# Optimization experiments

Measured on AMD Instinct MI355X. Metric: run time of the kernel, lower is better.

The kernel has to match this reference:

```python
import jax, jax.numpy as jnp
import numpy as np

D_MODEL = 256
N_HEAD = 8
D_FF = 1024
B = 8
N_PER = 4096
NQ = B * N_PER
L = 16
NEG_INF = -1e9
EPS = 1e-5


def layer_norm(x, g, b):
    mu = jnp.mean(x, axis=-1, keepdims=True)
    var = jnp.mean(jnp.square(x - mu), axis=-1, keepdims=True)
    return (x - mu) * jax.lax.rsqrt(var + EPS) * g + b


def setup_inputs() -> dict:
    key = jax.random.key(0)
    ks = jax.random.split(key, 20)
    s = 1.0 / np.sqrt(D_MODEL)
    sf = 1.0 / np.sqrt(D_FF)
    inp = {
        "src": jax.random.normal(ks[0], (NQ, D_MODEL), jnp.float32),
        "pos": jax.random.normal(ks[1], (NQ, D_MODEL), jnp.float32),
        # per-batch-relative neighbor indices in [-1, N_PER); -1 == invalid/padded
        "index_pair": jax.random.randint(ks[2], (NQ, L), 0, N_PER + 1, jnp.int32) - 1,
        "query_batch_cnt": jnp.full((B,), N_PER, jnp.int32),
        "key_batch_cnt": jnp.full((B,), N_PER, jnp.int32),
        "index_pair_batch": (jnp.arange(NQ, dtype=jnp.int32) // N_PER).astype(jnp.int32),
        "Wq": jax.random.normal(ks[3], (D_MODEL, D_MODEL), jnp.float32) * s,
        "bq": jnp.zeros((D_MODEL,), jnp.float32),
        "Wk": jax.random.normal(ks[4], (D_MODEL, D_MODEL), jnp.float32) * s,
        "bk": jnp.zeros((D_MODEL,), jnp.float32),
        "Wv": jax.random.normal(ks[5], (D_MODEL, D_MODEL), jnp.float32) * s,
        "bv": jnp.zeros((D_MODEL,), jnp.float32),
        "Wo": jax.random.normal(ks[6], (D_MODEL, D_MODEL), jnp.float32) * s,
        "bo": jnp.zeros((D_MODEL,), jnp.float32),
        "W1": jax.random.normal(ks[7], (D_MODEL, D_FF), jnp.float32) * s,
        "b1": jnp.zeros((D_FF,), jnp.float32),
        "W2": jax.random.normal(ks[8], (D_FF, D_MODEL), jnp.float32) * sf,
        "b2": jnp.zeros((D_MODEL,), jnp.float32),
        "g1": jnp.ones((D_MODEL,), jnp.float32),
        "be1": jnp.zeros((D_MODEL,), jnp.float32),
        "g2": jnp.ones((D_MODEL,), jnp.float32),
        "be2": jnp.zeros((D_MODEL,), jnp.float32),
    }
    return inp


def local_attn(q, k, v, index_pair, key_batch_cnt, index_pair_batch,
               Wq, bq, Wk, bk, Wv, bv, Wo, bo):
    H, hd = N_HEAD, D_MODEL // N_HEAD
    scale = 1.0 / np.sqrt(hd)
    qh = (q @ Wq + bq).reshape(NQ, H, hd) * scale        # [Nq,H,hd]
    kh = (k @ Wk + bk).reshape(NQ, H, hd)                # [Nk,H,hd] (Nk==Nq)
    vh = (v @ Wv + bv).reshape(NQ, H, hd)
    # start offset of each batch's keys in the stacked key tensor
    offs = jnp.cumsum(key_batch_cnt) - key_batch_cnt      # [B]
    valid = index_pair >= 0                               # [Nq,L]
    gidx = jnp.where(valid, index_pair + offs[index_pair_batch][:, None], 0)
    k_g = kh[gidx]                                        # [Nq,L,H,hd]
    v_g = vh[gidx]                                        # [Nq,L,H,hd]
    logits = jnp.einsum('nhd,nlhd->nhl', qh, k_g)         # [Nq,H,L]
    logits = jnp.where(valid[:, None, :], logits, NEG_INF)
    attn = jax.nn.softmax(logits, axis=-1)
    out = jnp.einsum('nhl,nlhd->nhd', attn, v_g).reshape(NQ, D_MODEL)
    return out @ Wo + bo


def reference(src, pos, index_pair, query_batch_cnt, key_batch_cnt, index_pair_batch,
              Wq, bq, Wk, bk, Wv, bv, Wo, bo, W1, b1, W2, b2, g1, be1, g2, be2):
    # forward_post (normalize_before=False), dropout==0 (eval)
    qk = src + pos
    src2 = local_attn(qk, qk, src, index_pair, key_batch_cnt, index_pair_batch,
                      Wq, bq, Wk, bk, Wv, bv, Wo, bo)
    x = layer_norm(src + src2, g1, be1)
    ff = jax.nn.relu(x @ W1 + b1) @ W2 + b2
    return layer_norm(x + ff, g2, be2)
```

## Files before the change

### kernel.cpp

```cpp
#include <hip/hip_runtime.h>
#include <hip/hip_bf16.h>
#include <cstdint>
#include <cstddef>

#define NQ_ 32768
#define DM_ 256
#define DFF_ 1024
#define LNB_ 16
#define NB_ 8

typedef __attribute__((ext_vector_type(4))) float f32x4;
typedef __attribute__((ext_vector_type(8))) short s16x8;

__device__ __forceinline__ float bf2f(ushort u) {
    union { unsigned int i; float f; } c; c.i = ((unsigned int)u) << 16; return c.f;
}
__device__ __forceinline__ ushort f2bf(float f) {
    union { float f; unsigned int i; } c; c.f = f;
    unsigned int x = c.i;
    return (ushort)((x + 0x7fffu + ((x >> 16) & 1u)) >> 16);
}


__global__ __launch_bounds__(256) void prep_qk(const float* __restrict__ src, const float* __restrict__ pos,
                                               ushort* __restrict__ qkb, ushort* __restrict__ srcb) {
    int i = (blockIdx.x * 256 + threadIdx.x) * 4;
    float4 s = *(const float4*)(src + i);
    float4 p = *(const float4*)(pos + i);
    ushort4 a, b;
    a.x = f2bf(s.x + p.x); a.y = f2bf(s.y + p.y); a.z = f2bf(s.z + p.z); a.w = f2bf(s.w + p.w);
    b.x = f2bf(s.x);       b.y = f2bf(s.y);       b.z = f2bf(s.z);       b.w = f2bf(s.w);
    *(ushort4*)(qkb + i) = a;
    *(ushort4*)(srcb + i) = b;
}

__global__ __launch_bounds__(256) void prep_weights(const float* __restrict__ Wq, const float* __restrict__ Wk,
                                                    const float* __restrict__ Wv, const float* __restrict__ Wo,
                                                    const float* __restrict__ W1, const float* __restrict__ W2,
                                                    const int* __restrict__ kbc,
                                                    const float* __restrict__ bq, const float* __restrict__ bk,
                                                    ushort* __restrict__ WqT, ushort* __restrict__ WkT,
                                                    ushort* __restrict__ WvT, ushort* __restrict__ WoT,
                                                    ushort* __restrict__ W1T, ushort* __restrict__ W2T,
                                                    int* __restrict__ offs, float* __restrict__ bias2) {
    const int b = blockIdx.x;
    const int t = threadIdx.x;
    if (b == 3072) {
        if (t == 0) { int a = 0; for (int i = 0; i < NB_; ++i) { offs[i] = a; a += kbc[i]; } }
        bias2[t] = bq[t];
        bias2[256 + t] = bk[t];
        return;
    }
    const float* W; ushort* Wt; int base, ks, ns;
    if (b < 1024) {
        const int sec = b >> 8;
        W  = sec == 0 ? Wq  : sec == 1 ? Wk  : sec == 2 ? Wv  : Wo;
        Wt = sec == 0 ? WqT : sec == 1 ? WkT : sec == 2 ? WvT : WoT;
        base = (b & 255) * 256; ks = 8; ns = 8;
    } else if (b < 2048) {
        W = W1; Wt = W1T; base = (b - 1024) * 256; ks = 8; ns = 10;
    } else {
        W = W2; Wt = W2T; base = (b - 2048) * 256; ks = 10; ns = 8;
    }
    const int i = base + t;
    const int n = i >> ks, k = i & ((1 << ks) - 1);
    Wt[i] = f2bf(W[(k << ns) + n]);
}


__device__ __forceinline__ void gld_lds16(const ushort* g, ushort* l) {
    __builtin_amdgcn_global_load_lds((const __attribute__((address_space(1))) void*)g,
                                     (__attribute__((address_space(3))) void*)l, 16, 0, 0);
}

template <bool RELU>
__global__ __launch_bounds__(256) void gemm_kernel(const ushort* __restrict__ A, const ushort* __restrict__ Bt,
                                                   const float* __restrict__ bias, ushort* __restrict__ C,
                                                   int M, int N, int K, float alpha) {
    __shared__ __align__(16) ushort As[2 * 128 * 32];
    __shared__ __align__(16) ushort Bs[2 * 128 * 32];
    const int tid = threadIdx.x;
    const int lane = tid & 63;
    const int wave = tid >> 6;
    const int wr = wave >> 1, wc = wave & 1;

    const int b = (int)(blockIdx.y * gridDim.x + blockIdx.x);
    const int idx = b >> 3;
    const int xt = (b & 7) * 32 + (idx & 31);
    const int yt = idx >> 5;
    const long m0 = (long)xt * 128;
    const long n0 = (long)yt * 128;

    f32x4 acc[4][4] = {};

    const int c0 = tid, c1 = tid + 256;
    const int ar0 = c0 >> 2, ac0 = c0 & 3;
    const int ar1 = c1 >> 2, ac1 = c1 & 3;
    const int as0 = (ac0 ^ ((ar0 >> 1) & 3)) * 8;
    const int as1 = (ac1 ^ ((ar1 >> 1) & 3)) * 8;
    const int la = lane & 15;
    const int sx = ((lane >> 4) ^ ((la >> 1) & 3)) * 8;

    const ushort* Ar0 = A + (m0 + ar0) * K + as0;
    const ushort* Ar1 = A + (m0 + ar1) * K + as1;
    const ushort* Br0 = Bt + (n0 + ar0) * K + as0;
    const ushort* Br1 = Bt + (n0 + ar1) * K + as1;

    const int nt = K >> 5;
    int boff = 0;
    gld_lds16(Ar0, As + c0 * 8);
    gld_lds16(Ar1, As + c1 * 8);
    gld_lds16(Br0, Bs + c0 * 8);
    gld_lds16(Br1, Bs + c1 * 8);

    for (int t = 0; t < nt; ++t) {
        if (t + 1 < nt) {
            const int kt = (t + 1) << 5;
            const int nb = boff ^ 4096;
            gld_lds16(Ar0 + kt, As + nb + c0 * 8);
            gld_lds16(Ar1 + kt, As + nb + c1 * 8);
            gld_lds16(Br0 + kt, Bs + nb + c0 * 8);
            gld_lds16(Br1 + kt, Bs + nb + c1 * 8);
            asm volatile("s_waitcnt vmcnt(4)" ::: "memory");
        } else {
            asm volatile("s_waitcnt vmcnt(0)" ::: "memory");
        }
        __builtin_amdgcn_s_barrier();
        s16x8 af[4], bfr[4];
#pragma unroll
        for (int m = 0; m < 4; ++m)
            af[m] = *(const s16x8*)(As + boff + (wr * 64 + m * 16 + la) * 32 + sx);
#pragma unroll
        for (int n = 0; n < 4; ++n)
            bfr[n] = *(const s16x8*)(Bs + boff + (wc * 64 + n * 16 + la) * 32 + sx);
        asm volatile("s_waitcnt lgkmcnt(0)" ::: "memory");
        __builtin_amdgcn_s_barrier();
#pragma unroll
        for (int m = 0; m < 4; ++m)
#pragma unroll
            for (int n = 0; n < 4; ++n)
                acc[m][n] = __builtin_amdgcn_mfma_f32_16x16x32_bf16(af[m], bfr[n], acc[m][n], 0, 0, 0);
        boff ^= 4096;
    }

#pragma unroll
    for (int n = 0; n < 4; ++n) {
        const long col = n0 + wc * 64 + n * 16 + la;
        const float bv = bias[col];
#pragma unroll
        for (int m = 0; m < 4; ++m) {
#pragma unroll
            for (int j = 0; j < 4; ++j) {
                const long row = m0 + wr * 64 + m * 16 + (lane >> 4) * 4 + j;
                float r = (acc[m][n][j] + bv) * alpha;
                if (RELU) r = fmaxf(r, 0.f);
                C[row * N + col] = f2bf(r);
            }
        }
    }
}


template <bool F32OUT>
__global__ __launch_bounds__(256) void gemm_ln_kernel(const ushort* __restrict__ A, const ushort* __restrict__ Bt,
                                                      const float* __restrict__ bias,
                                                      const ushort* __restrict__ resid,
                                                      const float* __restrict__ g, const float* __restrict__ be,
                                                      void* __restrict__ outv, int K) {
    __shared__ __align__(16) ushort As[64 * 32];
    __shared__ __align__(16) ushort Bs[256 * 32];
    __shared__ float red_s[4][64];
    __shared__ float red_q[4][64];
    const int tid = threadIdx.x;
    const int lane = tid & 63;
    const int wave = tid >> 6;
    const long m0 = (long)blockIdx.x * 64;

    const int ca = tid;
    const ushort* Arow = A + (m0 + (ca >> 2)) * K + ((ca & 3) ^ ((ca >> 3) & 3)) * 8;
    const ushort* Brow[4];
#pragma unroll
    for (int i = 0; i < 4; ++i) {
        const int cb = tid + 256 * i;
        Brow[i] = Bt + (long)(cb >> 2) * K + ((cb & 3) ^ ((cb >> 3) & 3)) * 8;
    }
    const int la = lane & 15;
    const int sx = ((lane >> 4) ^ ((la >> 1) & 3)) * 8;

    f32x4 acc[4][4] = {};

    for (int kt = 0; kt < K; kt += 32) {
        gld_lds16(Arow + kt, As + ca * 8);
#pragma unroll
        for (int i = 0; i < 4; ++i)
            gld_lds16(Brow[i] + kt, Bs + (tid + 256 * i) * 8);
        __syncthreads();
        s16x8 af[4], bfr[4];
#pragma unroll
        for (int m = 0; m < 4; ++m)
            af[m] = *(const s16x8*)(As + (m * 16 + la) * 32 + sx);
#pragma unroll
        for (int n = 0; n < 4; ++n)
            bfr[n] = *(const s16x8*)(Bs + (wave * 64 + n * 16 + la) * 32 + sx);
#pragma unroll
        for (int m = 0; m < 4; ++m)
#pragma unroll
            for (int n = 0; n < 4; ++n)
                acc[m][n] = __builtin_amdgcn_mfma_f32_16x16x32_bf16(af[m], bfr[n], acc[m][n], 0, 0, 0);
        __syncthreads();
    }

    const int rg4 = (lane >> 4) * 4;
    float bv[4];
#pragma unroll
    for (int n = 0; n < 4; ++n) bv[n] = bias[wave * 64 + n * 16 + la];

#pragma unroll
    for (int m = 0; m < 4; ++m) {
#pragma unroll
        for (int j = 0; j < 4; ++j) {
            const int lr = m * 16 + rg4 + j;
            float s = 0.f, q = 0.f;
#pragma unroll
            for (int n = 0; n < 4; ++n) {
                const int col = wave * 64 + n * 16 + la;
                float v = acc[m][n][j] + bv[n] + bf2f(resid[(m0 + lr) * DM_ + col]);
                acc[m][n][j] = v;
                s += v; q += v * v;
            }
#pragma unroll
            for (int mk = 1; mk < 16; mk <<= 1) { s += __shfl_xor(s, mk); q += __shfl_xor(q, mk); }
            if (la == 0) { red_s[wave][lr] = s; red_q[wave][lr] = q; }
        }
    }
    __syncthreads();

    float gv[4], bev[4];
#pragma unroll
    for (int n = 0; n < 4; ++n) {
        const int col = wave * 64 + n * 16 + la;
        gv[n] = g[col]; bev[n] = be[col];
    }
#pragma unroll
    for (int m = 0; m < 4; ++m) {
#pragma unroll
        for (int j = 0; j < 4; ++j) {
            const int lr = m * 16 + rg4 + j;
            const float s = red_s[0][lr] + red_s[1][lr] + red_s[2][lr] + red_s[3][lr];
            const float q = red_q[0][lr] + red_q[1][lr] + red_q[2][lr] + red_q[3][lr];
            const float mu = s * (1.f / 256.f);
            const float rsig = rsqrtf(q * (1.f / 256.f) - mu * mu + 1e-5f);
#pragma unroll
            for (int n = 0; n < 4; ++n) {
                const int col = wave * 64 + n * 16 + la;
                const float r = (acc[m][n][j] - mu) * rsig * gv[n] + bev[n];
                if (F32OUT) ((float*)outv)[(m0 + lr) * DM_ + col] = r;
                else        ((ushort*)outv)[(m0 + lr) * DM_ + col] = f2bf(r);
            }
        }
    }
}


__global__ __launch_bounds__(256, 4) void attn_kernel(const ushort* __restrict__ QKb,
                                                      const ushort* __restrict__ Vb, const int* __restrict__ ipair,
                                                      const int* __restrict__ ipb, const int* __restrict__ offs,
                                                      ushort* __restrict__ Ob) {
    const int blk = (blockIdx.x & 7) * (NQ_ / 8 / 8) + (blockIdx.x >> 3);
    const int lane = threadIdx.x & 63;
    const int n = blk * 8 + (threadIdx.x >> 6) * 2 + (lane >> 5);
    const size_t hoff = (size_t)(lane & 31) * 8;

    float q[8];
    {
        s16x8 v = *(const s16x8*)(QKb + (size_t)n * 512 + hoff);
#pragma unroll
        for (int e = 0; e < 8; ++e) q[e] = bf2f((ushort)v[e]);
    }
    const int off = offs[ipb[n]];
    int gi[LNB_];
    float lg[LNB_];
#pragma unroll
    for (int j = 0; j < LNB_; ++j) {
        const int ip = ipair[n * LNB_ + j];
        const int g = ip >= 0 ? ip + off : 0;
        gi[j] = g;
        s16x8 v = *(const s16x8*)(QKb + (size_t)g * 512 + 256 + hoff);
        float p = 0.f;
#pragma unroll
        for (int e = 0; e < 8; ++e)
            p = fmaf(q[e], bf2f((ushort)v[e]), p);
        p += __shfl_xor(p, 1);
        p += __shfl_xor(p, 2);
        lg[j] = ip >= 0 ? p * 0.17677669529663688f : -1e9f;
    }
    float mx = lg[0];
#pragma unroll
    for (int j = 1; j < LNB_; ++j) mx = fmaxf(mx, lg[j]);
    float sum = 0.f, pw[LNB_];
#pragma unroll
    for (int j = 0; j < LNB_; ++j) { pw[j] = __expf(lg[j] - mx); sum += pw[j]; }
    const float inv = 1.f / sum;

    float acc[8] = {};
#pragma unroll
    for (int j = 0; j < LNB_; ++j) {
        s16x8 v = *(const s16x8*)(Vb + (size_t)gi[j] * DM_ + hoff);
        const float w = pw[j] * inv;
#pragma unroll
        for (int e = 0; e < 8; ++e)
            acc[e] = fmaf(w, bf2f((ushort)v[e]), acc[e]);
    }
    s16x8 o;
#pragma unroll
    for (int e = 0; e < 8; ++e) o[e] = (short)f2bf(acc[e]);
    *(s16x8*)(Ob + (size_t)n * DM_ + hoff) = o;
}


extern "C" void kernel_launch(void* const* d_in, const int* in_sizes, int n_in,
                              void* d_out, int out_size, void* d_ws, size_t ws_size,
                              hipStream_t stream) {
    const float* src = (const float*)d_in[0];
    const float* pos = (const float*)d_in[1];
    const int* ipair = (const int*)d_in[2];
    const int* kbc   = (const int*)d_in[4];
    const int* ipb   = (const int*)d_in[5];
    const float* Wq = (const float*)d_in[6];  const float* bq = (const float*)d_in[7];
    const float* Wk = (const float*)d_in[8];  const float* bk = (const float*)d_in[9];
    const float* Wv = (const float*)d_in[10]; const float* bv = (const float*)d_in[11];
    const float* Wo = (const float*)d_in[12]; const float* bo = (const float*)d_in[13];
    const float* W1 = (const float*)d_in[14]; const float* b1 = (const float*)d_in[15];
    const float* W2 = (const float*)d_in[16]; const float* b2 = (const float*)d_in[17];
    const float* g1 = (const float*)d_in[18]; const float* be1 = (const float*)d_in[19];
    const float* g2 = (const float*)d_in[20]; const float* be2 = (const float*)d_in[21];

    char* ws = (char*)d_ws;
    const size_t SB = (size_t)NQ_ * DM_ * 2;
    ushort* qkb  = (ushort*)(ws);
    ushort* srcb = (ushort*)(ws + SB);
    ushort* QKb  = (ushort*)(ws + 2 * SB);
    ushort* Vb   = (ushort*)(ws + 4 * SB);
    ushort* hb   = (ushort*)(ws);
    ushort* attno = qkb;
    ushort* xb    = Vb;
    char* wb = ws + 6 * SB;
    ushort* WqT = (ushort*)(wb);
    ushort* WkT = (ushort*)(wb + 131072);
    ushort* WvT = (ushort*)(wb + 262144);
    ushort* WoT = (ushort*)(wb + 393216);
    ushort* W1T = (ushort*)(wb + 524288);
    ushort* W2T = (ushort*)(wb + 1048576);
    int* offs   = (int*)(wb + 1572864);
    float* bias2 = (float*)(wb + 1572864 + 64);

    prep_weights<<<3073, 256, 0, stream>>>(Wq, Wk, Wv, Wo, W1, W2, kbc, bq, bk,
                                           WqT, WkT, WvT, WoT, W1T, W2T, offs, bias2);
    prep_qk<<<NQ_ * DM_ / 4 / 256, 256, 0, stream>>>(src, pos, qkb, srcb);

    dim3 gqk(NQ_ / 128, 512 / 128);
    dim3 g256(NQ_ / 128, DM_ / 128);
    dim3 gff1(NQ_ / 128, DFF_ / 128);
    gemm_kernel<false><<<gqk, 256, 0, stream>>>(qkb, WqT, bias2, QKb, NQ_, 512, DM_, 1.f);
    gemm_kernel<false><<<g256, 256, 0, stream>>>(srcb, WvT, bv, Vb, NQ_, DM_, DM_, 1.f);
    attn_kernel<<<NQ_ / 8, 256, 0, stream>>>(QKb, Vb, ipair, ipb, offs, attno);
    gemm_ln_kernel<false><<<NQ_ / 64, 256, 0, stream>>>(attno, WoT, bo, srcb, g1, be1, (void*)xb, DM_);
    gemm_kernel<true><<<gff1, 256, 0, stream>>>(xb, W1T, b1, hb, NQ_, DFF_, DM_, 1.f);
    gemm_ln_kernel<true><<<NQ_ / 64, 256, 0, stream>>>(hb, W2T, b2, xb, g2, be2, d_out, DFF_);
}
```

Measured before the change: 182.3 us.

## Fuse FFN up-projection, ReLU, down-projection and LayerNorm into one kernel

Replaces the separate W1 GEMM and W2 GEMM+LayerNorm kernels with a single kernel that keeps a 64-row tile of x in LDS, computes the hidden activations in 256-column chunks into LDS, and immediately accumulates them against W2. This removes the write and read of the 32768x1024 bf16 hidden tensor in global memory and one launch. In exchange each block re-streams all of W1 and W2 through a small LDS buffer with a sync per k-step and no double buffering, uses about 48KB of LDS, and holds two 64-row accumulator sets in registers, which may limit occupancy.

```diff
diff --git a/kernel.cpp b/kernel.cpp
--- a/kernel.cpp
+++ b/kernel.cpp
@@ -262,6 +262,151 @@
 }
 
 
+__global__ __launch_bounds__(256, 2) void ff_fused_kernel(const ushort* __restrict__ X,
+                                                          const ushort* __restrict__ W1T,
+                                                          const float* __restrict__ b1,
+                                                          const ushort* __restrict__ W2T,
+                                                          const float* __restrict__ b2,
+                                                          const float* __restrict__ g, const float* __restrict__ be,
+                                                          float* __restrict__ out) {
+    __shared__ __align__(16) ushort Xs[64 * 256];
+    __shared__ __align__(16) ushort Hs[64 * 256];
+    __shared__ __align__(16) ushort Bs[256 * 32];
+    const int tid = threadIdx.x;
+    const int lane = tid & 63;
+    const int wave = tid >> 6;
+    const long m0 = (long)blockIdx.x * 64;
+
+    const int la = lane & 15;
+    const int sx = ((lane >> 4) ^ ((la >> 1) & 3)) * 8;
+    const int rg4 = (lane >> 4) * 4;
+
+#pragma unroll
+    for (int i = 0; i < 8; ++i) {
+        const int c = tid + 256 * i;
+        const int row = c >> 5, a = c & 31, kt = a >> 2, rel = a & 3;
+        gld_lds16(X + (m0 + row) * DM_ + kt * 32 + ((rel ^ ((row >> 1) & 3)) * 8), Xs + c * 8);
+    }
+
+    const int nrow[4] = { (tid + 0) >> 2, (tid + 256) >> 2, (tid + 512) >> 2, (tid + 768) >> 2 };
+    int bsw[4];
+#pragma unroll
+    for (int i = 0; i < 4; ++i) {
+        const int cb = tid + 256 * i;
+        bsw[i] = ((cb & 3) ^ ((nrow[i] >> 1) & 3)) * 8;
+    }
+
+    f32x4 acc2[4][4] = {};
+
+    for (int c = 0; c < 4; ++c) {
+        const int cbase = c * 256;
+        f32x4 acc1[4][4] = {};
+        for (int kt = 0; kt < 8; ++kt) {
+#pragma unroll
+            for (int i = 0; i < 4; ++i)
+                gld_lds16(W1T + (long)(cbase + nrow[i]) * DM_ + kt * 32 + bsw[i], Bs + (tid + 256 * i) * 8);
+            __syncthreads();
+            s16x8 af[4], bfr[4];
+#pragma unroll
+            for (int m = 0; m < 4; ++m)
+                af[m] = *(const s16x8*)(Xs + (m * 16 + la) * 256 + kt * 32 + sx);
+#pragma unroll
+            for (int n = 0; n < 4; ++n)
+                bfr[n] = *(const s16x8*)(Bs + (wave * 64 + n * 16 + la) * 32 + sx);
+#pragma unroll
+            for (int m = 0; m < 4; ++m)
+#pragma unroll
+                for (int n = 0; n < 4; ++n)
+                    acc1[m][n] = __builtin_amdgcn_mfma_f32_16x16x32_bf16(af[m], bfr[n], acc1[m][n], 0, 0, 0);
+            __syncthreads();
+        }
+#pragma unroll
+        for (int n = 0; n < 4; ++n) {
+            const int ccl = wave * 64 + n * 16 + la;
+            const int kt2 = ccl >> 5, rel2 = (ccl >> 3) & 3, w8 = ccl & 7;
+            const float b1v = b1[cbase + ccl];
+#pragma unroll
+            for (int m = 0; m < 4; ++m) {
+#pragma unroll
+                for (int j = 0; j < 4; ++j) {
+                    const int lr = m * 16 + rg4 + j;
+                    const float v = fmaxf(acc1[m][n][j] + b1v, 0.f);
+                    Hs[lr * 256 + kt2 * 32 + ((rel2 ^ ((lr >> 1) & 3)) * 8) + w8] = f2bf(v);
+                }
+            }
+        }
+        __syncthreads();
+        for (int kt = 0; kt < 8; ++kt) {
+#pragma unroll
+            for (int i = 0; i < 4; ++i)
+                gld_lds16(W2T + (long)nrow[i] * DFF_ + cbase + kt * 32 + bsw[i], Bs + (tid + 256 * i) * 8);
+            __syncthreads();
+            s16x8 af[4], bfr[4];
+#pragma unroll
+            for (int m = 0; m < 4; ++m)
+                af[m] = *(const s16x8*)(Hs + (m * 16 + la) * 256 + kt * 32 + sx);
+#pragma unroll
+            for (int n = 0; n < 4; ++n)
+                bfr[n] = *(const s16x8*)(Bs + (wave * 64 + n * 16 + la) * 32 + sx);
+#pragma unroll
+            for (int m = 0; m < 4; ++m)
+#pragma unroll
+                for (int n = 0; n < 4; ++n)
+                    acc2[m][n] = __builtin_amdgcn_mfma_f32_16x16x32_bf16(af[m], bfr[n], acc2[m][n], 0, 0, 0);
+            __syncthreads();
+        }
+    }
+
+    float* red = (float*)Bs;
+    float b2v[4];
+#pragma unroll
+    for (int n = 0; n < 4; ++n) b2v[n] = b2[wave * 64 + n * 16 + la];
+
+#pragma unroll
+    for (int m = 0; m < 4; ++m) {
+#pragma unroll
+        for (int j = 0; j < 4; ++j) {
+            const int lr = m * 16 + rg4 + j;
+            float s = 0.f, q = 0.f;
+#pragma unroll
+            for (int n = 0; n < 4; ++n) {
+                const int col = wave * 64 + n * 16 + la;
+                float v = acc2[m][n][j] + b2v[n] + bf2f(X[(m0 + lr) * DM_ + col]);
+                acc2[m][n][j] = v;
+                s += v; q += v * v;
+            }
+#pragma unroll
+            for (int mk = 1; mk < 16; mk <<= 1) { s += __shfl_xor(s, mk); q += __shfl_xor(q, mk); }
+            if (la == 0) { red[wave * 64 + lr] = s; red[256 + wave * 64 + lr] = q; }
+        }
+    }
+    __syncthreads();
+
+    float gv[4], bev[4];
+#pragma unroll
+    for (int n = 0; n < 4; ++n) {
+        const int col = wave * 64 + n * 16 + la;
+        gv[n] = g[col]; bev[n] = be[col];
+    }
+#pragma unroll
+    for (int m = 0; m < 4; ++m) {
+#pragma unroll
+        for (int j = 0; j < 4; ++j) {
+            const int lr = m * 16 + rg4 + j;
+            const float s = red[lr] + red[64 + lr] + red[128 + lr] + red[192 + lr];
+            const float q = red[256 + lr] + red[320 + lr] + red[384 + lr] + red[448 + lr];
+            const float mu = s * (1.f / 256.f);
+            const float rsig = rsqrtf(q * (1.f / 256.f) - mu * mu + 1e-5f);
+#pragma unroll
+            for (int n = 0; n < 4; ++n) {
+                const int col = wave * 64 + n * 16 + la;
+                out[(m0 + lr) * DM_ + col] = (acc2[m][n][j] - mu) * rsig * gv[n] + bev[n];
+            }
+        }
+    }
+}
+
+
 __global__ __launch_bounds__(256, 4) void attn_kernel(const ushort* __restrict__ QKb,
                                                       const ushort* __restrict__ Vb, const int* __restrict__ ipair,
                                                       const int* __restrict__ ipb, const int* __restrict__ offs,
@@ -341,7 +486,6 @@
     ushort* srcb = (ushort*)(ws + SB);
     ushort* QKb  = (ushort*)(ws + 2 * SB);
     ushort* Vb   = (ushort*)(ws + 4 * SB);
-    ushort* hb   = (ushort*)(ws);
     ushort* attno = qkb;
     ushort* xb    = Vb;
     char* wb = ws + 6 * SB;
@@ -360,11 +504,9 @@
 
     dim3 gqk(NQ_ / 128, 512 / 128);
     dim3 g256(NQ_ / 128, DM_ / 128);
-    dim3 gff1(NQ_ / 128, DFF_ / 128);
     gemm_kernel<false><<<gqk, 256, 0, stream>>>(qkb, WqT, bias2, QKb, NQ_, 512, DM_, 1.f);
     gemm_kernel<false><<<g256, 256, 0, stream>>>(srcb, WvT, bv, Vb, NQ_, DM_, DM_, 1.f);
     attn_kernel<<<NQ_ / 8, 256, 0, stream>>>(QKb, Vb, ipair, ipb, offs, attno);
     gemm_ln_kernel<false><<<NQ_ / 64, 256, 0, stream>>>(attno, WoT, bo, srcb, g1, be1, (void*)xb, DM_);
-    gemm_kernel<true><<<gff1, 256, 0, stream>>>(xb, W1T, b1, hb, NQ_, DFF_, DM_, 1.f);
-    gemm_ln_kernel<true><<<NQ_ / 64, 256, 0, stream>>>(hb, W2T, b2, xb, g2, be2, d_out, DFF_);
-}
+    ff_fused_kernel<<<NQ_ / 64, 256, 0, stream>>>(xb, W1T, b1, W2T, b2, g2, be2, (float*)d_out);
+}
```

Measured after the change: 183.6 us. No clear change (+0.7%).
